# Performance work log

Hardware: AMD Instinct MI355X
Metric: run time of the kernel (lower is better)

The kernel has to match this reference:

```python
import jax, jax.numpy as jnp
import numpy as np

B, T, I, H, O = 2048, 72, 200, 200, 53
EPS = 1e-5


def _gru_layer(x, h0, Wih, Whh, bih, bhh):
    """PyTorch-convention GRU. x: [B,T,I], h0: [B,H]. Gate order: r, z, n."""
    xW = jnp.einsum('bti,gi->btg', x, Wih) + bih  # [B,T,3H] precomputed input proj

    def step(h, xw):
        hw = h @ Whh.T + bhh                       # [B,3H]
        xr, xz, xn = jnp.split(xw, 3, axis=-1)
        hr, hz, hn = jnp.split(hw, 3, axis=-1)
        r = jax.nn.sigmoid(xr + hr)
        z = jax.nn.sigmoid(xz + hz)
        n = jnp.tanh(xn + r * hn)
        h_new = (1.0 - z) * n + z * h
        return h_new, h_new

    hT, ys = jax.lax.scan(step, h0, jnp.swapaxes(xW, 0, 1))  # ys: [T,B,H]
    return jnp.swapaxes(ys, 0, 1), hT


def setup_inputs() -> dict:
    key = jax.random.key(0)
    ks = jax.random.split(key, 16)
    s = 0.05
    inp = {
        'encoded': jax.random.normal(ks[0], (B, I), dtype=jnp.float32),
        'hidden_1': jnp.zeros((1, B, H), dtype=jnp.float32),
        'hidden_2': jnp.zeros((1, B, H), dtype=jnp.float32),
        'hidden_3': jnp.zeros((1, B, H), dtype=jnp.float32),
        # BatchNorm1d (eval mode: running stats)
        'bn_gamma': jnp.ones((I,), jnp.float32),
        'bn_beta': jnp.zeros((I,), jnp.float32),
        'bn_mean': jnp.zeros((I,), jnp.float32),
        'bn_var': jnp.ones((I,), jnp.float32),
        'fc_in_W': jax.random.normal(ks[1], (H, I), jnp.float32) * s,
        'fc_in_b': jnp.zeros((H,), jnp.float32),
        'Wih1': jax.random.normal(ks[2], (3 * H, I), jnp.float32) * s,
        'Whh1': jax.random.normal(ks[3], (3 * H, H), jnp.float32) * s,
        'bih1': jnp.zeros((3 * H,), jnp.float32),
        'bhh1': jnp.zeros((3 * H,), jnp.float32),
        'Wih2': jax.random.normal(ks[4], (3 * H, H), jnp.float32) * s,
        'Whh2': jax.random.normal(ks[5], (3 * H, H), jnp.float32) * s,
        'bih2': jnp.zeros((3 * H,), jnp.float32),
        'bhh2': jnp.zeros((3 * H,), jnp.float32),
        'Wih3': jax.random.normal(ks[6], (3 * H, H), jnp.float32) * s,
        'Whh3': jax.random.normal(ks[7], (3 * H, H), jnp.float32) * s,
        'bih3': jnp.zeros((3 * H,), jnp.float32),
        'bhh3': jnp.zeros((3 * H,), jnp.float32),
        'fc_out_W': jax.random.normal(ks[8], (O, H), jnp.float32) * s,
        'fc_out_b': jnp.zeros((O,), jnp.float32),
    }
    return inp


def reference(encoded, hidden_1, hidden_2, hidden_3, bn_gamma, bn_beta, bn_mean,
              bn_var, fc_in_W, fc_in_b, Wih1, Whh1, bih1, bhh1, Wih2, Whh2,
              bih2, bhh2, Wih3, Whh3, bih3, bhh3, fc_out_W, fc_out_b):
    # BatchNorm1d (eval) -> Linear -> ReLU
    xh = (encoded - bn_mean) * jax.lax.rsqrt(bn_var + EPS) * bn_gamma + bn_beta
    emb = jax.nn.relu(xh @ fc_in_W.T + fc_in_b)              # [B,H]
    embedded = jnp.broadcast_to(emb[:, None, :], (B, T, H))  # repeat over T

    out1, h1 = _gru_layer(embedded, hidden_1[0], Wih1, Whh1, bih1, bhh1)
    out2, h2 = _gru_layer(out1, hidden_2[0], Wih2, Whh2, bih2, bhh2)
    out3, h3 = _gru_layer(out2, hidden_3[0], Wih3, Whh3, bih3, bhh3)

    out = jnp.einsum('bth,oh->bto', out3, fc_out_W) + fc_out_b  # [B,T,O]
    out = jax.nn.relu(jax.nn.sigmoid(out))
    return out, h1[None], h2[None], h3[None]
```

## Files before the change

kernel.cpp:

```cpp
#include <hip/hip_runtime.h>

typedef _Float16 half8 __attribute__((ext_vector_type(8)));
typedef float f32x4 __attribute__((ext_vector_type(4)));

namespace {
constexpr int kB = 2048;
constexpr int kT = 72;
constexpr int kI = 200;
constexpr int kH = 200;
constexpr int kO = 53;
constexpr int kG = 600;
constexpr int BT = 8;
constexpr int NWG = kB / BT;
constexpr int MT = 38;
constexpr int KS = 7;
constexpr int GSTR = 18;

constexpr int XW1    = 0;
constexpr int WIH1T  = 1228800;
constexpr int FCINT  = 1348800;
constexpr int F0     = 1388800;
constexpr int FSZ    = 68096;
constexpr int FHEAD  = F0 + 5 * FSZ;
constexpr int PERM   = MT * KS * 64;

constexpr int OH1 = kB * kT * kO;
constexpr int OH2 = OH1 + kB * kH;
constexpr int OH3 = OH2 + kB * kH;
}

__device__ __forceinline__ float sig_(float x) { return 1.0f / (1.0f + __expf(-x)); }
__device__ __forceinline__ float tanh_(float x) {
    return 1.0f - 2.0f / (__expf(2.0f * x) + 1.0f);
}

__device__ __forceinline__ void barx() {
    asm volatile("s_waitcnt lgkmcnt(0)\n\ts_barrier" ::: "memory");
}

__device__ __forceinline__ void store_fb(_Float16* fb, int n, int j, float v) {
    int ks = j >> 5, r = j & 31;
    fb[((ks << 6) + ((r >> 3) << 4) + n) * 8 + (r & 7)] = (_Float16)v;
}


__global__ __launch_bounds__(256) void prep_transpose2(
    const float* __restrict__ Wih1, const float* __restrict__ fciW,
    float* __restrict__ ws) {
    int idx = blockIdx.x * 256 + threadIdx.x;
    if (idx < 120000) {
        int k = idx / kG, c = idx - k * kG;
        ws[WIH1T + idx] = Wih1[c * kI + k];
    } else {
        int i = idx - 120000;
        if (i < 40000) {
            int k = i / kH, h = i - k * kH;
            ws[FCINT + i] = fciW[h * kI + k];
        }
    }
}

__global__ __launch_bounds__(256) void prep_frags(
    const float* __restrict__ Whh1, const float* __restrict__ Wih2,
    const float* __restrict__ Whh2, const float* __restrict__ Wih3,
    const float* __restrict__ Whh3, const float* __restrict__ fcoW,
    float* __restrict__ ws) {
    int idx = blockIdx.x * 256 + threadIdx.x;
    const float* src; int R; long long dstHalf; int rem;
    if (idx < 5 * PERM) {
        int m = idx / PERM; rem = idx - m * PERM;
        switch (m) {
            case 0: src = Whh1; break;
            case 1: src = Wih2; break;
            case 2: src = Whh2; break;
            case 3: src = Wih3; break;
            default: src = Whh3; break;
        }
        R = kG; dstHalf = 2LL * (F0 + m * FSZ);
    } else {
        rem = idx - 5 * PERM;
        if (rem >= 4 * KS * 64) return;
        src = fcoW; R = kO; dstHalf = 2LL * FHEAD;
    }
    int lane = rem & 63;
    int tmp = rem >> 6;
    int ks = tmp % KS;
    int mt = tmp / KS;
    int row = mt * 16 + (lane & 15);
    int k0 = ks * 32 + (lane >> 4) * 8;
    half8 v;
    #pragma unroll
    for (int j = 0; j < 8; ++j) {
        int k = k0 + j;
        v[j] = (_Float16)((row < R && k < kH) ? src[row * kH + k] : 0.0f);
    }
    *(half8*)((_Float16*)ws + dstHalf + (long long)rem * 8) = v;
}

__global__ __launch_bounds__(256) void prep_input(
    const float* __restrict__ enc,
    const float* __restrict__ bn_g, const float* __restrict__ bn_b,
    const float* __restrict__ bn_m, const float* __restrict__ bn_v,
    const float* __restrict__ fcib, const float* __restrict__ bih1,
    float* ws) {
    __shared__ float xh[kI];
    __shared__ float emb[kH];
    const int b = blockIdx.x, tid = threadIdx.x;
    const float* fcInT = ws + FCINT;
    const float* Wih1T = ws + WIH1T;
    if (tid < kI) {
        float x = enc[b * kI + tid];
        xh[tid] = (x - bn_m[tid]) * rsqrtf(bn_v[tid] + 1e-5f) * bn_g[tid] + bn_b[tid];
    }
    __syncthreads();
    if (tid < kH) {
        float s = fcib[tid];
        for (int k = 0; k < kI; ++k) s = fmaf(xh[k], fcInT[k * kH + tid], s);
        emb[tid] = fmaxf(s, 0.0f);
    }
    __syncthreads();
    for (int c = tid; c < kG; c += 256) {
        float s = bih1[c];
        for (int k = 0; k < kH; ++k) s = fmaf(emb[k], Wih1T[k * kG + c], s);
        ws[XW1 + b * kG + c] = s;
    }
}

__global__ __launch_bounds__(1024, 4) void gru_main(
    const float* __restrict__ ws,
    const float* __restrict__ h1in, const float* __restrict__ h2in,
    const float* __restrict__ h3in,
    const float* __restrict__ bhh1,
    const float* __restrict__ bih2, const float* __restrict__ bhh2,
    const float* __restrict__ bih3, const float* __restrict__ bhh3,
    const float* __restrict__ fcob,
    float* __restrict__ out) {
    __shared__ float xwL[kG * BT];
    __shared__ __align__(16) _Float16 fb1[KS * 64 * 8];
    __shared__ __align__(16) _Float16 fb2[KS * 64 * 8];
    __shared__ __align__(16) _Float16 fb3[KS * 64 * 8];
    __shared__ float Gs[608 * GSTR];
    __shared__ float Gns[208 * GSTR];
    __shared__ float bias[9 * kH];
    __shared__ float hb[64];

    const int tid = threadIdx.x, wv = tid >> 6, ln = tid & 63;
    const int lb = ln >> 4, lr = ln & 15;
    const int b0 = blockIdx.x * BT;

    {
        float4* f1 = (float4*)fb1;
        float4* f2 = (float4*)fb2;
        float4* f3 = (float4*)fb3;
        const float4 z4 = {0.f, 0.f, 0.f, 0.f};
        for (int i = tid; i < KS * 64 * 8 * 2 / 16; i += 1024) {
            f1[i] = z4; f2[i] = z4; f3[i] = z4;
        }
    }
    for (int i = tid; i < kG * BT; i += 1024) {
        int n = i / kG, j = i - n * kG;
        float v = ws[XW1 + (b0 + n) * kG + j];
        if (j < 2 * kH) v += bhh1[j];
        xwL[j * BT + n] = v;
    }
    for (int i = tid; i < 9 * kH; i += 1024) {
        int c = i / kH, j = i - c * kH;
        float v;
        switch (c) {
            case 0:  v = bhh1[2 * kH + j]; break;
            case 1:  v = bih2[j] + bhh2[j]; break;
            case 2:  v = bih2[kH + j] + bhh2[kH + j]; break;
            case 3:  v = bih2[2 * kH + j]; break;
            case 4:  v = bhh2[2 * kH + j]; break;
            case 5:  v = bih3[j] + bhh3[j]; break;
            case 6:  v = bih3[kH + j] + bhh3[kH + j]; break;
            case 7:  v = bih3[2 * kH + j]; break;
            default: v = bhh3[2 * kH + j]; break;
        }
        bias[i] = v;
    }
    if (tid < 64) hb[tid] = (tid < kO) ? fcob[tid] : 0.0f;
    __syncthreads();

    float h1r[2], h2r[2], h3r[2];
    #pragma unroll
    for (int s = 0; s < 2; ++s) {
        int idx = tid + s * 1024;
        if (idx < BT * kH) {
            int n = idx & 7, j = idx >> 3;
            h1r[s] = h1in[(b0 + n) * kH + j];
            h2r[s] = h2in[(b0 + n) * kH + j];
            h3r[s] = h3in[(b0 + n) * kH + j];
            store_fb(fb1, n, j, h1r[s]);
            store_fb(fb2, n, j, h2r[s]);
            store_fb(fb3, n, j, h3r[s]);
        } else { h1r[s] = h2r[s] = h3r[s] = 0.0f; }
    }
    __syncthreads();

    const half8* WFhh1 = (const half8*)(ws + F0);
    const half8* WFih2 = (const half8*)(ws + F0 + FSZ);
    const half8* WFhh2 = (const half8*)(ws + F0 + 2 * FSZ);
    const half8* WFih3 = (const half8*)(ws + F0 + 3 * FSZ);
    const half8* WFhh3 = (const half8*)(ws + F0 + 4 * FSZ);
    const half8* WFhead = (const half8*)(ws + FHEAD);

    for (int t = 0; t < kT; ++t) {
        {
            half8 bf[KS];
            #pragma unroll
            for (int ks = 0; ks < KS; ++ks)
                bf[ks] = *(const half8*)(fb1 + (ks * 64 + ln) * 8);
            for (int mt = wv; mt < MT; mt += 16) {
                const half8* wp = WFhh1 + (mt * KS) * 64 + ln;
                f32x4 acc = {0.f, 0.f, 0.f, 0.f};
                #pragma unroll
                for (int ks = 0; ks < KS; ++ks)
                    acc = __builtin_amdgcn_mfma_f32_16x16x32_f16(wp[ks * 64], bf[ks], acc, 0, 0, 0);
                int row = mt * 16 + lb * 4;
                #pragma unroll
                for (int rg = 0; rg < 4; ++rg) Gs[(row + rg) * GSTR + lr] = acc[rg];
            }
        }
        barx();
        #pragma unroll
        for (int s = 0; s < 2; ++s) {
            int idx = tid + s * 1024;
            if (idx < BT * kH) {
                int n = idx & 7, j = idx >> 3;
                float r  = sig_(xwL[j * BT + n]            + Gs[j * GSTR + n]);
                float z  = sig_(xwL[(kH + j) * BT + n]     + Gs[(kH + j) * GSTR + n]);
                float nn = tanh_(xwL[(2 * kH + j) * BT + n] + r * (Gs[(2 * kH + j) * GSTR + n] + bias[j]));
                h1r[s] = (1.0f - z) * nn + z * h1r[s];
                store_fb(fb1, n, j, h1r[s]);
            }
        }
        barx();
        {
            half8 bx[KS], bh[KS];
            #pragma unroll
            for (int ks = 0; ks < KS; ++ks) {
                bx[ks] = *(const half8*)(fb1 + (ks * 64 + ln) * 8);
                bh[ks] = *(const half8*)(fb2 + (ks * 64 + ln) * 8);
            }
            for (int mt = wv; mt < MT; mt += 16) {
                const half8* wpx = WFih2 + (mt * KS) * 64 + ln;
                const half8* wph = WFhh2 + (mt * KS) * 64 + ln;
                f32x4 ax = {0.f, 0.f, 0.f, 0.f}, ah = {0.f, 0.f, 0.f, 0.f};
                #pragma unroll
                for (int ks = 0; ks < KS; ++ks) {
                    ax = __builtin_amdgcn_mfma_f32_16x16x32_f16(wpx[ks * 64], bx[ks], ax, 0, 0, 0);
                    ah = __builtin_amdgcn_mfma_f32_16x16x32_f16(wph[ks * 64], bh[ks], ah, 0, 0, 0);
                }
                int row = mt * 16 + lb * 4;
                if (mt < 25) {
                    #pragma unroll
                    for (int rg = 0; rg < 4; ++rg) Gs[(row + rg) * GSTR + lr] = ax[rg] + ah[rg];
                } else {
                    #pragma unroll
                    for (int rg = 0; rg < 4; ++rg) {
                        Gs[(row + rg) * GSTR + lr] = ax[rg];
                        Gns[(row - 400 + rg) * GSTR + lr] = ah[rg];
                    }
                }
            }
        }
        barx();
        #pragma unroll
        for (int s = 0; s < 2; ++s) {
            int idx = tid + s * 1024;
            if (idx < BT * kH) {
                int n = idx & 7, j = idx >> 3;
                float r  = sig_(Gs[j * GSTR + n]            + bias[kH + j]);
                float z  = sig_(Gs[(kH + j) * GSTR + n]     + bias[2 * kH + j]);
                float nn = tanh_(Gs[(2 * kH + j) * GSTR + n] + bias[3 * kH + j]
                                 + r * (Gns[j * GSTR + n]   + bias[4 * kH + j]));
                h2r[s] = (1.0f - z) * nn + z * h2r[s];
                store_fb(fb2, n, j, h2r[s]);
            }
        }
        barx();
        {
            half8 bx[KS], bh[KS];
            #pragma unroll
            for (int ks = 0; ks < KS; ++ks) {
                bx[ks] = *(const half8*)(fb2 + (ks * 64 + ln) * 8);
                bh[ks] = *(const half8*)(fb3 + (ks * 64 + ln) * 8);
            }
            for (int mt = wv; mt < MT; mt += 16) {
                const half8* wpx = WFih3 + (mt * KS) * 64 + ln;
                const half8* wph = WFhh3 + (mt * KS) * 64 + ln;
                f32x4 ax = {0.f, 0.f, 0.f, 0.f}, ah = {0.f, 0.f, 0.f, 0.f};
                #pragma unroll
                for (int ks = 0; ks < KS; ++ks) {
                    ax = __builtin_amdgcn_mfma_f32_16x16x32_f16(wpx[ks * 64], bx[ks], ax, 0, 0, 0);
                    ah = __builtin_amdgcn_mfma_f32_16x16x32_f16(wph[ks * 64], bh[ks], ah, 0, 0, 0);
                }
                int row = mt * 16 + lb * 4;
                if (mt < 25) {
                    #pragma unroll
                    for (int rg = 0; rg < 4; ++rg) Gs[(row + rg) * GSTR + lr] = ax[rg] + ah[rg];
                } else {
                    #pragma unroll
                    for (int rg = 0; rg < 4; ++rg) {
                        Gs[(row + rg) * GSTR + lr] = ax[rg];
                        Gns[(row - 400 + rg) * GSTR + lr] = ah[rg];
                    }
                }
            }
        }
        barx();
        #pragma unroll
        for (int s = 0; s < 2; ++s) {
            int idx = tid + s * 1024;
            if (idx < BT * kH) {
                int n = idx & 7, j = idx >> 3;
                float r  = sig_(Gs[j * GSTR + n]            + bias[5 * kH + j]);
                float z  = sig_(Gs[(kH + j) * GSTR + n]     + bias[6 * kH + j]);
                float nn = tanh_(Gs[(2 * kH + j) * GSTR + n] + bias[7 * kH + j]
                                 + r * (Gns[j * GSTR + n]   + bias[8 * kH + j]));
                h3r[s] = (1.0f - z) * nn + z * h3r[s];
                store_fb(fb3, n, j, h3r[s]);
            }
        }
        barx();
        if (wv < 4) {
            half8 bf[KS];
            #pragma unroll
            for (int ks = 0; ks < KS; ++ks)
                bf[ks] = *(const half8*)(fb3 + (ks * 64 + ln) * 8);
            const half8* wp = WFhead + (wv * KS) * 64 + ln;
            f32x4 acc = {0.f, 0.f, 0.f, 0.f};
            #pragma unroll
            for (int ks = 0; ks < KS; ++ks)
                acc = __builtin_amdgcn_mfma_f32_16x16x32_f16(wp[ks * 64], bf[ks], acc, 0, 0, 0);
            if (lr < BT) {
                int o0 = wv * 16 + lb * 4;
                int obase = (b0 + lr) * (kT * kO) + t * kO;
                #pragma unroll
                for (int rg = 0; rg < 4; ++rg) {
                    int o = o0 + rg;
                    if (o < kO) out[obase + o] = sig_(acc[rg] + hb[o]);
                }
            }
        }
        barx();
    }

    #pragma unroll
    for (int s = 0; s < 2; ++s) {
        int idx = tid + s * 1024;
        if (idx < BT * kH) {
            Gs[idx] = h1r[s];
            Gs[1600 + idx] = h2r[s];
            Gs[3200 + idx] = h3r[s];
        }
    }
    __syncthreads();
    for (int i = tid; i < BT * kH; i += 1024) {
        int n = i / kH, j = i - n * kH;
        int src = j * BT + n;
        out[OH1 + (b0 + n) * kH + j] = Gs[src];
        out[OH2 + (b0 + n) * kH + j] = Gs[1600 + src];
        out[OH3 + (b0 + n) * kH + j] = Gs[3200 + src];
    }
}

extern "C" void kernel_launch(void* const* d_in, const int* in_sizes, int n_in,
                              void* d_out, int out_size, void* d_ws, size_t ws_size,
                              hipStream_t stream) {
    (void)in_sizes; (void)n_in; (void)out_size; (void)ws_size;
    const float* enc  = (const float*)d_in[0];
    const float* h1in = (const float*)d_in[1];
    const float* h2in = (const float*)d_in[2];
    const float* h3in = (const float*)d_in[3];
    const float* bn_g = (const float*)d_in[4];
    const float* bn_b = (const float*)d_in[5];
    const float* bn_m = (const float*)d_in[6];
    const float* bn_v = (const float*)d_in[7];
    const float* fciW = (const float*)d_in[8];
    const float* fcib = (const float*)d_in[9];
    const float* Wih1 = (const float*)d_in[10];
    const float* Whh1 = (const float*)d_in[11];
    const float* bih1 = (const float*)d_in[12];
    const float* bhh1 = (const float*)d_in[13];
    const float* Wih2 = (const float*)d_in[14];
    const float* Whh2 = (const float*)d_in[15];
    const float* bih2 = (const float*)d_in[16];
    const float* bhh2 = (const float*)d_in[17];
    const float* Wih3 = (const float*)d_in[18];
    const float* Whh3 = (const float*)d_in[19];
    const float* bih3 = (const float*)d_in[20];
    const float* bhh3 = (const float*)d_in[21];
    const float* fcoW = (const float*)d_in[22];
    const float* fcob = (const float*)d_in[23];
    float* ws  = (float*)d_ws;
    float* out = (float*)d_out;

    hipLaunchKernelGGL(prep_transpose2, dim3(625), dim3(256), 0, stream, Wih1, fciW, ws);
    hipLaunchKernelGGL(prep_frags, dim3(340), dim3(256), 0, stream,
                       Whh1, Wih2, Whh2, Wih3, Whh3, fcoW, ws);
    hipLaunchKernelGGL(prep_input, dim3(kB), dim3(256), 0, stream,
                       enc, bn_g, bn_b, bn_m, bn_v, fcib, bih1, ws);
    hipLaunchKernelGGL(gru_main, dim3(NWG), dim3(1024), 0, stream,
                       ws, h1in, h2in, h3in, bhh1, bih2, bhh2, bih3, bhh3, fcob, out);
}
```

Measured before the change: 1.151 ms.

## Prefetch next-stage MFMA weight fragments across barriers and cache head weights in registers

Each wave now loads its first weight tile for the next GEMM stage into registers right after the preceding barrier, so the global/L2 fetch overlaps the elementwise gate computation. The head projection weights are kept in registers for the whole time loop instead of being reloaded every step. The last K-slice is loaded only by lanes below 16 and zero-filled for the rest, which skips loads that contribute nothing. This raises register pressure under launch_bounds(1024,4), which may cause spills.

```diff
diff --git a/kernel.cpp b/kernel.cpp
--- a/kernel.cpp
+++ b/kernel.cpp
@@ -125,6 +125,13 @@
         ws[XW1 + b * kG + c] = s;
     }
 }
+
+#define LDW(dst, WB, mt) do { \
+    const half8* _p = (WB) + ((mt) * KS) * 64 + ln; \
+    _Pragma("unroll") \
+    for (int _k = 0; _k < KS - 1; ++_k) (dst)[_k] = _p[_k * 64]; \
+    if (lo) (dst)[KS - 1] = _p[(KS - 1) * 64]; else (dst)[KS - 1] = z8; \
+  } while (0)
 
 __global__ __launch_bounds__(1024, 4) void gru_main(
     const float* __restrict__ ws,
@@ -147,6 +154,10 @@
     const int tid = threadIdx.x, wv = tid >> 6, ln = tid & 63;
     const int lb = ln >> 4, lr = ln & 15;
     const int b0 = blockIdx.x * BT;
+    const bool lo = (ln < 16);
+    half8 z8;
+    #pragma unroll
+    for (int j = 0; j < 8; ++j) z8[j] = (_Float16)0.0f;
 
     {
         float4* f1 = (float4*)fb1;
@@ -205,24 +216,43 @@
     const half8* WFhh3 = (const half8*)(ws + F0 + 4 * FSZ);
     const half8* WFhead = (const half8*)(ws + FHEAD);
 
+    half8 p1[KS], p2x[KS], p2h[KS], p3x[KS], p3h[KS], whd[KS];
+    LDW(p1, WFhh1, wv);
+    if (wv < 4) LDW(whd, WFhead, wv);
+
     for (int t = 0; t < kT; ++t) {
         {
             half8 bf[KS];
             #pragma unroll
             for (int ks = 0; ks < KS; ++ks)
                 bf[ks] = *(const half8*)(fb1 + (ks * 64 + ln) * 8);
-            for (int mt = wv; mt < MT; mt += 16) {
+            {
+                f32x4 acc = {0.f, 0.f, 0.f, 0.f};
+                #pragma unroll
+                for (int ks = 0; ks < KS; ++ks)
+                    acc = __builtin_amdgcn_mfma_f32_16x16x32_f16(p1[ks], bf[ks], acc, 0, 0, 0);
+                int row = wv * 16 + lb * 4;
+                #pragma unroll
+                for (int rg = 0; rg < 4; ++rg) Gs[(row + rg) * GSTR + lr] = acc[rg];
+            }
+            for (int mt = wv + 16; mt < MT; mt += 16) {
                 const half8* wp = WFhh1 + (mt * KS) * 64 + ln;
+                half8 w[KS];
+                #pragma unroll
+                for (int ks = 0; ks < KS - 1; ++ks) w[ks] = wp[ks * 64];
+                if (lo) w[KS - 1] = wp[(KS - 1) * 64]; else w[KS - 1] = z8;
                 f32x4 acc = {0.f, 0.f, 0.f, 0.f};
                 #pragma unroll
                 for (int ks = 0; ks < KS; ++ks)
-                    acc = __builtin_amdgcn_mfma_f32_16x16x32_f16(wp[ks * 64], bf[ks], acc, 0, 0, 0);
+                    acc = __builtin_amdgcn_mfma_f32_16x16x32_f16(w[ks], bf[ks], acc, 0, 0, 0);
                 int row = mt * 16 + lb * 4;
                 #pragma unroll
                 for (int rg = 0; rg < 4; ++rg) Gs[(row + rg) * GSTR + lr] = acc[rg];
             }
         }
         barx();
+        LDW(p2x, WFih2, wv);
+        LDW(p2h, WFhh2, wv);
         #pragma unroll
         for (int s = 0; s < 2; ++s) {
             int idx = tid + s * 1024;
@@ -243,14 +273,30 @@
                 bx[ks] = *(const half8*)(fb1 + (ks * 64 + ln) * 8);
                 bh[ks] = *(const half8*)(fb2 + (ks * 64 + ln) * 8);
             }
-            for (int mt = wv; mt < MT; mt += 16) {
+            {
+                f32x4 ax = {0.f, 0.f, 0.f, 0.f}, ah = {0.f, 0.f, 0.f, 0.f};
+                #pragma unroll
+                for (int ks = 0; ks < KS; ++ks) {
+                    ax = __builtin_amdgcn_mfma_f32_16x16x32_f16(p2x[ks], bx[ks], ax, 0, 0, 0);
+                    ah = __builtin_amdgcn_mfma_f32_16x16x32_f16(p2h[ks], bh[ks], ah, 0, 0, 0);
+                }
+                int row = wv * 16 + lb * 4;
+                #pragma unroll
+                for (int rg = 0; rg < 4; ++rg) Gs[(row + rg) * GSTR + lr] = ax[rg] + ah[rg];
+            }
+            for (int mt = wv + 16; mt < MT; mt += 16) {
                 const half8* wpx = WFih2 + (mt * KS) * 64 + ln;
                 const half8* wph = WFhh2 + (mt * KS) * 64 + ln;
+                half8 wx[KS], wh[KS];
+                #pragma unroll
+                for (int ks = 0; ks < KS - 1; ++ks) { wx[ks] = wpx[ks * 64]; wh[ks] = wph[ks * 64]; }
+                if (lo) { wx[KS - 1] = wpx[(KS - 1) * 64]; wh[KS - 1] = wph[(KS - 1) * 64]; }
+                else    { wx[KS - 1] = z8; wh[KS - 1] = z8; }
                 f32x4 ax = {0.f, 0.f, 0.f, 0.f}, ah = {0.f, 0.f, 0.f, 0.f};
                 #pragma unroll
                 for (int ks = 0; ks < KS; ++ks) {
-                    ax = __builtin_amdgcn_mfma_f32_16x16x32_f16(wpx[ks * 64], bx[ks], ax, 0, 0, 0);
-                    ah = __builtin_amdgcn_mfma_f32_16x16x32_f16(wph[ks * 64], bh[ks], ah, 0, 0, 0);
+                    ax = __builtin_amdgcn_mfma_f32_16x16x32_f16(wx[ks], bx[ks], ax, 0, 0, 0);
+                    ah = __builtin_amdgcn_mfma_f32_16x16x32_f16(wh[ks], bh[ks], ah, 0, 0, 0);
                 }
                 int row = mt * 16 + lb * 4;
                 if (mt < 25) {
@@ -266,6 +312,8 @@
             }
         }
         barx();
+        LDW(p3x, WFih3, wv);
+        LDW(p3h, WFhh3, wv);
         #pragma unroll
         for (int s = 0; s < 2; ++s) {
             int idx = tid + s * 1024;
@@ -287,14 +335,30 @@
                 bx[ks] = *(const half8*)(fb2 + (ks * 64 + ln) * 8);
                 bh[ks] = *(const half8*)(fb3 + (ks * 64 + ln) * 8);
             }
-            for (int mt = wv; mt < MT; mt += 16) {
+            {
+                f32x4 ax = {0.f, 0.f, 0.f, 0.f}, ah = {0.f, 0.f, 0.f, 0.f};
+                #pragma unroll
+                for (int ks = 0; ks < KS; ++ks) {
+                    ax = __builtin_amdgcn_mfma_f32_16x16x32_f16(p3x[ks], bx[ks], ax, 0, 0, 0);
+                    ah = __builtin_amdgcn_mfma_f32_16x16x32_f16(p3h[ks], bh[ks], ah, 0, 0, 0);
+                }
+                int row = wv * 16 + lb * 4;
+                #pragma unroll
+                for (int rg = 0; rg < 4; ++rg) Gs[(row + rg) * GSTR + lr] = ax[rg] + ah[rg];
+            }
+            for (int mt = wv + 16; mt < MT; mt += 16) {
                 const half8* wpx = WFih3 + (mt * KS) * 64 + ln;
                 const half8* wph = WFhh3 + (mt * KS) * 64 + ln;
+                half8 wx[KS], wh[KS];
+                #pragma unroll
+                for (int ks = 0; ks < KS - 1; ++ks) { wx[ks] = wpx[ks * 64]; wh[ks] = wph[ks * 64]; }
+                if (lo) { wx[KS - 1] = wpx[(KS - 1) * 64]; wh[KS - 1] = wph[(KS - 1) * 64]; }
+                else    { wx[KS - 1] = z8; wh[KS - 1] = z8; }
                 f32x4 ax = {0.f, 0.f, 0.f, 0.f}, ah = {0.f, 0.f, 0.f, 0.f};
                 #pragma unroll
                 for (int ks = 0; ks < KS; ++ks) {
-                    ax = __builtin_amdgcn_mfma_f32_16x16x32_f16(wpx[ks * 64], bx[ks], ax, 0, 0, 0);
-                    ah = __builtin_amdgcn_mfma_f32_16x16x32_f16(wph[ks * 64], bh[ks], ah, 0, 0, 0);
+                    ax = __builtin_amdgcn_mfma_f32_16x16x32_f16(wx[ks], bx[ks], ax, 0, 0, 0);
+                    ah = __builtin_amdgcn_mfma_f32_16x16x32_f16(wh[ks], bh[ks], ah, 0, 0, 0);
                 }
                 int row = mt * 16 + lb * 4;
                 if (mt < 25) {
@@ -310,6 +374,7 @@
             }
         }
         barx();
+        LDW(p1, WFhh1, wv);
         #pragma unroll
         for (int s = 0; s < 2; ++s) {
             int idx = tid + s * 1024;
@@ -329,11 +394,10 @@
             #pragma unroll
             for (int ks = 0; ks < KS; ++ks)
                 bf[ks] = *(const half8*)(fb3 + (ks * 64 + ln) * 8);
-            const half8* wp = WFhead + (wv * KS) * 64 + ln;
             f32x4 acc = {0.f, 0.f, 0.f, 0.f};
             #pragma unroll
             for (int ks = 0; ks < KS; ++ks)
-                acc = __builtin_amdgcn_mfma_f32_16x16x32_f16(wp[ks * 64], bf[ks], acc, 0, 0, 0);
+                acc = __builtin_amdgcn_mfma_f32_16x16x32_f16(whd[ks], bf[ks], acc, 0, 0, 0);
             if (lr < BT) {
                 int o0 = wv * 16 + lb * 4;
                 int obase = (b0 + lr) * (kT * kO) + t * kO;
```

Result: slower. 2.111 ms (+83.5%).
